# Kernel optimization log

Hardware: AMD Instinct MI355X
Metric: run time of the kernel (lower is better)

The kernel has to match this reference:

```python
import jax, jax.numpy as jnp
import numpy as np

N = 100000   # nodes
E = 1600000  # edges
F = 128      # in = out features
BN_EPS = 1e-5


def setup_inputs() -> dict:
    key = jax.random.key(0)
    ks = jax.random.split(key, 20)
    s = 1.0 / np.sqrt(F)
    inp = {
        "x": jax.random.normal(ks[0], (N, F), dtype=jnp.float32),
        "edge_index": jax.random.randint(ks[1], (2, E), 0, N, dtype=jnp.int64),
        "edge_type": jax.random.randint(ks[2], (E,), 0, 2, dtype=jnp.int64),
        # self-loop linear
        "w_sl": jax.random.normal(ks[3], (F, F), dtype=jnp.float32) * s,
        "b_sl": jnp.zeros((F,), dtype=jnp.float32),
        # GIN MLP for relation 0 (edge_type==0)
        "w1_n": jax.random.normal(ks[4], (F, F), dtype=jnp.float32) * s,
        "b1_n": jnp.zeros((F,), dtype=jnp.float32),
        "gamma_n": jnp.ones((F,), dtype=jnp.float32),
        "beta_n": jnp.zeros((F,), dtype=jnp.float32),
        "w2_n": jax.random.normal(ks[5], (F, F), dtype=jnp.float32) * s,
        "b2_n": jnp.zeros((F,), dtype=jnp.float32),
        # GIN MLP for relation 1 (edge_type==1)
        "w1_d": jax.random.normal(ks[6], (F, F), dtype=jnp.float32) * s,
        "b1_d": jnp.zeros((F,), dtype=jnp.float32),
        "gamma_d": jnp.ones((F,), dtype=jnp.float32),
        "beta_d": jnp.zeros((F,), dtype=jnp.float32),
        "w2_d": jax.random.normal(ks[7], (F, F), dtype=jnp.float32) * s,
        "b2_d": jnp.zeros((F,), dtype=jnp.float32),
        # gate linear: 3F -> F
        "w_gat": jax.random.normal(ks[8], (F, 3 * F), dtype=jnp.float32) * (1.0 / np.sqrt(3 * F)),
        "b_gat": jnp.zeros((F,), dtype=jnp.float32),
    }
    return inp


def _gin_branch(x, src, dst, mask, w1, b1, gamma, beta, w2, b2):
    # masked gather-scatter: equivalent to selecting edge columns with edge_type==r
    msg = x[src] * mask[:, None]                         # [E, F]
    agg = jax.ops.segment_sum(msg, dst, num_segments=N)  # [N, F]
    h = agg + x                                          # (1 + eps)*x with eps=0
    h = h @ w1.T + b1
    # BatchNorm1d, training-mode batch statistics (biased variance)
    mu = jnp.mean(h, axis=0)
    var = jnp.var(h, axis=0)
    h = gamma * (h - mu) * jax.lax.rsqrt(var + BN_EPS) + beta
    h = jax.nn.relu(h)
    return h @ w2.T + b2


def reference(x, edge_index, edge_type, w_sl, b_sl,
              w1_n, b1_n, gamma_n, beta_n, w2_n, b2_n,
              w1_d, b1_d, gamma_d, beta_d, w2_d, b2_d,
              w_gat, b_gat):
    src, dst = edge_index[0], edge_index[1]
    mask_n = (edge_type == 0).astype(x.dtype)
    mask_d = (edge_type == 1).astype(x.dtype)

    x_new_x = x @ w_sl.T + b_sl
    x_new_n = _gin_branch(x, src, dst, mask_n, w1_n, b1_n, gamma_n, beta_n, w2_n, b2_n)
    x_new_d = _gin_branch(x, src, dst, mask_d, w1_d, b1_d, gamma_d, beta_d, w2_d, b2_d)

    cat = jnp.concatenate((x_new_x, x_new_n, x_new_d), axis=1)   # [N, 3F]
    gat_raw = jax.nn.softmax(cat @ w_gat.T + b_gat, axis=-1)     # [N, F]
    gat = jnp.cumsum(gat_raw, axis=-1)
    out = (x_new_x + x_new_n) * (1.0 - gat) + (x_new_x + x_new_n + jnp.flip(x_new_d, axis=1)) * gat
    return out
```

## Files before the change

kernel.cpp:

```cpp
#include <hip/hip_runtime.h>
#include <stdint.h>

#define FF 128
#define MFMA __builtin_amdgcn_mfma_f32_16x16x32_bf16

typedef __attribute__((ext_vector_type(8))) short bf8_t;
typedef __attribute__((ext_vector_type(4))) float f4_t;
typedef __attribute__((ext_vector_type(8))) uint16_t us8_t;

__device__ __forceinline__ uint16_t f2bf(float f) {
  union { float f; uint32_t u; } v; v.f = f;
  return (uint16_t)((v.u + 0x7fffu + ((v.u >> 16) & 1u)) >> 16);
}
__device__ __forceinline__ float bf2f(uint16_t h) {
  union { uint32_t u; float f; } v; v.u = ((uint32_t)h) << 16;
  return v.f;
}

__device__ __forceinline__ void g2lds16(const void* g, void* l) {
  __builtin_amdgcn_global_load_lds(
      (const __attribute__((address_space(1))) uint32_t*)g,
      (__attribute__((address_space(3))) uint32_t*)l, 16, 0, 0);
}

#define STAGE_W8(Wp)                                                           \
  do {                                                                         \
    _Pragma("unroll") for (int j_ = 0; j_ < 4; ++j_) {                         \
      int k_ = j_ * 8 + w;                                                     \
      int r_ = ((k_ & 1) << 6) + lane;                                         \
      int c_ = k_ >> 1;                                                        \
      g2lds16((const char*)(Wp) + (size_t)r_ * 256 + c_ * 16,                  \
              (char*)wlds + k_ * 1024);                                        \
    }                                                                          \
  } while (0)

#define STAGE2(Wp, Gp)                                                         \
  do {                                                                         \
    _Pragma("unroll") for (int j_ = 0; j_ < 8; ++j_) {                         \
      int k_ = j_ * 8 + w;                                                     \
      int cc_ = k_ & 31;                                                       \
      const char* sp_ = (j_ < 4) ? (const char*)(Wp) : (const char*)(Gp);      \
      int r_ = ((cc_ & 1) << 6) + lane;                                        \
      int c_ = cc_ >> 1;                                                       \
      g2lds16(sp_ + (size_t)r_ * 256 + c_ * 16, (char*)wlds + k_ * 1024);      \
    }                                                                          \
  } while (0)

#define WFRAG(s, t) (*(const bf8_t*)&wlds[((s)*4 + lg) * 1024 + ((t)*16 + lr) * 8])
#define GFRAG(s, t) \
  (*(const bf8_t*)&wlds[16384 + ((s)*4 + lg) * 1024 + ((t)*16 + lr) * 8])

__global__ __launch_bounds__(256) void cvt_w_k(
    const float* __restrict__ wsl, const float* __restrict__ w1n,
    const float* __restrict__ w2n, const float* __restrict__ w1d,
    const float* __restrict__ w2d, uint16_t* __restrict__ o) {
  int i = blockIdx.x * 256 + threadIdx.x;
  if (i >= 5 * 16384) return;
  int wsel = i >> 14, j = i & 16383;
  const float* p = (wsel == 0) ? wsl : (wsel == 1) ? w1n : (wsel == 2) ? w2n
                   : (wsel == 3) ? w1d : w2d;
  o[i] = f2bf(p[j]);
}

__global__ __launch_bounds__(256) void gatepre_k(
    const float* __restrict__ wgat, const float* __restrict__ wsl,
    const float* __restrict__ w2n, const float* __restrict__ w2d,
    uint16_t* __restrict__ G) {
  const int mat = blockIdx.x >> 3;
  const int jblk = blockIdx.x & 7;
  const float* A = wgat + mat * 128;
  const float* B = (mat == 0) ? wsl : (mat == 1) ? w2n : w2d;
  const int i = threadIdx.x & 127;
  const int jo = jblk * 16 + (threadIdx.x >> 7) * 8;
  float acc[8] = {0.f, 0.f, 0.f, 0.f, 0.f, 0.f, 0.f, 0.f};
#pragma unroll 4
  for (int k = 0; k < 128; ++k) {
    float a = A[(size_t)i * 384 + k];
    const float* br = B + (size_t)k * 128 + jo;
#pragma unroll
    for (int j = 0; j < 8; ++j) acc[j] = fmaf(a, br[j], acc[j]);
  }
  uint16_t* g = G + mat * 16384 + i * 128 + jo;
#pragma unroll
  for (int j = 0; j < 8; ++j) g[j] = f2bf(acc[j]);
}

__global__ void bgatp_k(const float* __restrict__ wgat, const float* __restrict__ b_sl,
                        const float* __restrict__ b2n, const float* __restrict__ b2d,
                        const float* __restrict__ bgat, float* __restrict__ bgp) {
  int i = threadIdx.x;
  float s = bgat[i];
  for (int k = 0; k < 128; ++k) {
    s += wgat[(size_t)i * 384 + k] * b_sl[k];
    s += wgat[(size_t)i * 384 + 128 + k] * b2n[k];
    s += wgat[(size_t)i * 384 + 256 + k] * b2d[k];
  }
  bgp[i] = s;
}

__global__ __launch_bounds__(256) void cvt_x_k(const float* __restrict__ x,
                                               uint16_t* __restrict__ xb, int n4) {
  int i = blockIdx.x * 256 + threadIdx.x;
  if (i >= n4) return;
  float4 v = ((const float4*)x)[i];
  uint2 o;
  o.x = ((uint32_t)f2bf(v.y) << 16) | f2bf(v.x);
  o.y = ((uint32_t)f2bf(v.w) << 16) | f2bf(v.z);
  ((uint2*)xb)[i] = o;
}

__global__ __launch_bounds__(256) void hist_k(const int* __restrict__ dst,
                                              const int* __restrict__ ety,
                                              int* __restrict__ hist, int E) {
  int i = blockIdx.x * 256 + threadIdx.x;
  if (i < E) atomicAdd(&hist[(dst[i] << 1) | ety[i]], 1);
}

__global__ __launch_bounds__(256) void scan1_k(const int* __restrict__ hist,
                                               int* __restrict__ off,
                                               int* __restrict__ bsum, int nbins) {
  int i = blockIdx.x * 256 + threadIdx.x;
  int v = (i < nbins) ? hist[i] : 0;
  int lane = threadIdx.x & 63, w = threadIdx.x >> 6;
  int s = v;
#pragma unroll
  for (int d = 1; d < 64; d <<= 1) {
    int o = __shfl_up(s, (unsigned)d, 64);
    if (lane >= d) s += o;
  }
  __shared__ int wsum[4];
  if (lane == 63) wsum[w] = s;
  __syncthreads();
  int add = 0;
  for (int k = 0; k < w; ++k) add += wsum[k];
  s += add;
  if (i < nbins) off[i] = s - v;
  if (threadIdx.x == 255) bsum[blockIdx.x] = s;
}

__global__ __launch_bounds__(1024) void scan2_k(int* __restrict__ bsum, int nb) {
  int t = threadIdx.x;
  int v = (t < nb) ? bsum[t] : 0;
  int lane = t & 63, w = t >> 6;
  int s = v;
#pragma unroll
  for (int d = 1; d < 64; d <<= 1) {
    int o = __shfl_up(s, (unsigned)d, 64);
    if (lane >= d) s += o;
  }
  __shared__ int ws[16];
  if (lane == 63) ws[w] = s;
  __syncthreads();
  int add = 0;
  for (int k = 0; k < w; ++k) add += ws[k];
  s += add;
  if (t < nb) bsum[t] = s - v;
}

__global__ __launch_bounds__(256) void scan3_k(int* __restrict__ off,
                                               int* __restrict__ ccur,
                                               const int* __restrict__ bsum,
                                               int nbins, int E) {
  int i = blockIdx.x * 256 + threadIdx.x;
  if (i < nbins) {
    int v = off[i] + bsum[blockIdx.x];
    off[i] = v;
    if ((i & 511) == 0) ccur[i >> 9] = v;
  }
  if (i == nbins) off[i] = E;
}

#define BK_EPT 16
__global__ __launch_bounds__(256) void bucketize_k(const int* __restrict__ src,
                                                   const int* __restrict__ dst,
                                                   const int* __restrict__ ety,
                                                   int* __restrict__ ccur,
                                                   uint32_t* __restrict__ bk,
                                                   int E, int nbuckets) {
  __shared__ int lhist[512];
  __shared__ int lbase[512];
  const int tid = threadIdx.x;
  const int base = blockIdx.x * (256 * BK_EPT);
  for (int j = tid; j < nbuckets; j += 256) lhist[j] = 0;
  __syncthreads();

  uint32_t pk[BK_EPT];
  uint32_t rk[BK_EPT];
#pragma unroll
  for (int j = 0; j < BK_EPT; ++j) {
    int i = base + j * 256 + tid;
    if (i < E) {
      int bin = (dst[i] << 1) | ety[i];
      int bucket = bin >> 9;
      int rank = atomicAdd(&lhist[bucket], 1);
      pk[j] = (uint32_t)src[i] | ((uint32_t)(bin & 511) << 17);
      rk[j] = (uint32_t)bucket | ((uint32_t)rank << 9);
    } else {
      rk[j] = 0xFFFFFFFFu;
    }
  }
  __syncthreads();
  for (int j = tid; j < nbuckets; j += 256) {
    int c = lhist[j];
    lbase[j] = c ? atomicAdd(&ccur[j], c) : 0;
  }
  __syncthreads();
#pragma unroll
  for (int j = 0; j < BK_EPT; ++j) {
    if (rk[j] != 0xFFFFFFFFu) {
      int bucket = (int)(rk[j] & 511u);
      int rank = (int)(rk[j] >> 9);
      bk[lbase[bucket] + rank] = pk[j];
    }
  }
}

__global__ __launch_bounds__(256) void sctfine_k(const int* __restrict__ off,
                                                 const uint32_t* __restrict__ bk,
                                                 int* __restrict__ ssrc, int nbins) {
  __shared__ int lcur[512];
  const int b = blockIdx.x;
  const int binbase = b << 9;
  const int binend = min(binbase + 512, nbins);
  for (int j = threadIdx.x; j < binend - binbase; j += 256)
    lcur[j] = off[binbase + j];
  __syncthreads();
  const int estart = off[binbase], eend = off[binend];
  for (int i = estart + (int)threadIdx.x; i < eend; i += 256) {
    uint32_t pk = bk[i];
    int pos = atomicAdd(&lcur[pk >> 17], 1);
    ssrc[pos] = (int)(pk & 0x1FFFFu);
  }
}

__global__ __launch_bounds__(256) void agg_k(const int* __restrict__ off,
                                             const int* __restrict__ ssrc,
                                             const uint16_t* __restrict__ xb,
                                             uint16_t* __restrict__ xanb,
                                             uint16_t* __restrict__ xadb, int nbins) {
  int wid = (blockIdx.x * 256 + threadIdx.x) >> 6;
  int lane = threadIdx.x & 63;
  if (wid >= nbins) return;
  const int q = lane >> 4, c = lane & 15;
  int e = off[wid], end = off[wid + 1];
  float acc[8] = {0.f, 0.f, 0.f, 0.f, 0.f, 0.f, 0.f, 0.f};

#define ACC8(v)                                                       \
  do {                                                                \
    union { uint32_t u; float f; } lo_, hi_;                          \
    lo_.u = (v).x << 16; hi_.u = (v).x & 0xffff0000u;                 \
    acc[0] += lo_.f; acc[1] += hi_.f;                                 \
    lo_.u = (v).y << 16; hi_.u = (v).y & 0xffff0000u;                 \
    acc[2] += lo_.f; acc[3] += hi_.f;                                 \
    lo_.u = (v).z << 16; hi_.u = (v).z & 0xffff0000u;                 \
    acc[4] += lo_.f; acc[5] += hi_.f;                                 \
    lo_.u = (v).w << 16; hi_.u = (v).w & 0xffff0000u;                 \
    acc[6] += lo_.f; acc[7] += hi_.f;                                 \
  } while (0)

  for (; e + 8 <= end; e += 8) {
    int s0 = ssrc[e + q];
    int s1 = ssrc[e + 4 + q];
    uint4 v0 = *(const uint4*)(xb + (size_t)s0 * FF + c * 8);
    uint4 v1 = *(const uint4*)(xb + (size_t)s1 * FF + c * 8);
    ACC8(v0);
    ACC8(v1);
  }
  for (; e + 4 <= end; e += 4) {
    int s0 = ssrc[e + q];
    uint4 v0 = *(const uint4*)(xb + (size_t)s0 * FF + c * 8);
    ACC8(v0);
  }
  int r = end - e;
  if (r > 0) {
    int s0 = ssrc[e + min(q, r - 1)];
    uint4 v0 = *(const uint4*)(xb + (size_t)s0 * FF + c * 8);
    if (q < r) ACC8(v0);
  }
#undef ACC8

#pragma unroll
  for (int j = 0; j < 8; ++j) {
    acc[j] += __shfl_xor(acc[j], 16, 64);
    acc[j] += __shfl_xor(acc[j], 32, 64);
  }
  const int n = wid >> 1;
  uint4 own = *(const uint4*)(xb + (size_t)n * FF + c * 8);
  {
    union { uint32_t u; float f; } lo_, hi_;
    lo_.u = own.x << 16; hi_.u = own.x & 0xffff0000u;
    acc[0] += lo_.f; acc[1] += hi_.f;
    lo_.u = own.y << 16; hi_.u = own.y & 0xffff0000u;
    acc[2] += lo_.f; acc[3] += hi_.f;
    lo_.u = own.z << 16; hi_.u = own.z & 0xffff0000u;
    acc[4] += lo_.f; acc[5] += hi_.f;
    lo_.u = own.w << 16; hi_.u = own.w & 0xffff0000u;
    acc[6] += lo_.f; acc[7] += hi_.f;
  }
  if (q == 0) {
    uint4 o;
    o.x = ((uint32_t)f2bf(acc[1]) << 16) | f2bf(acc[0]);
    o.y = ((uint32_t)f2bf(acc[3]) << 16) | f2bf(acc[2]);
    o.z = ((uint32_t)f2bf(acc[5]) << 16) | f2bf(acc[4]);
    o.w = ((uint32_t)f2bf(acc[7]) << 16) | f2bf(acc[6]);
    uint16_t* dstp = (wid & 1) ? xadb : xanb;
    *(uint4*)(dstp + (size_t)n * FF + c * 8) = o;
  }
}

__global__ __launch_bounds__(512) void gemm1_k(
    const uint16_t* __restrict__ xanb, const uint16_t* __restrict__ xadb,
    const uint16_t* __restrict__ wbf, const float* __restrict__ b1n,
    const float* __restrict__ b1d, uint16_t* __restrict__ h1n,
    uint16_t* __restrict__ h1d, float* __restrict__ gstats, int N) {
  __shared__ __align__(16) uint16_t wlds[16384];
  __shared__ float sstat[8][4][128];
  const int tid = threadIdx.x;
  const int lane = tid & 63, w = tid >> 6;
  const int lr = lane & 15, lg = lane >> 4;
  const int rowbase = blockIdx.x * 256 + w * 32;
  const int arow0 = min(rowbase + lr, N - 1);
  const int arow1 = min(rowbase + 16 + lr, N - 1);

  f4_t acc[2][8];
  const f4_t zz = {0.f, 0.f, 0.f, 0.f};
  bf8_t a0[4], a1[4];

  STAGE_W8(wbf + 16384);
#pragma unroll
  for (int s = 0; s < 4; ++s) {
    const int k0 = s * 32 + lg * 8;
    a0[s] = *(const bf8_t*)(xanb + (size_t)arow0 * FF + k0);
    a1[s] = *(const bf8_t*)(xanb + (size_t)arow1 * FF + k0);
  }
  __syncthreads();

#pragma unroll 1
  for (int gi = 0; gi < 2; ++gi) {
#pragma unroll
    for (int rg = 0; rg < 2; ++rg)
#pragma unroll
      for (int t = 0; t < 8; ++t) acc[rg][t] = zz;
#pragma unroll
    for (int s = 0; s < 4; ++s) {
#pragma unroll
      for (int t = 0; t < 8; ++t) {
        bf8_t b = WFRAG(s, t);
        acc[0][t] = MFMA(a0[s], b, acc[0][t], 0, 0, 0);
        acc[1][t] = MFMA(a1[s], b, acc[1][t], 0, 0, 0);
      }
    }
    const float* bp = gi ? b1d : b1n;
    uint16_t* hp = gi ? h1d : h1n;
#pragma unroll
    for (int t = 0; t < 8; ++t) {
      const int col = t * 16 + lr;
      const float b = bp[col];
      float sum = 0.f, ss = 0.f;
#pragma unroll
      for (int rg = 0; rg < 2; ++rg)
#pragma unroll
        for (int r = 0; r < 4; ++r) {
          const int row = rowbase + rg * 16 + lg * 4 + r;
          const float h = acc[rg][t][r] + b;
          if (row < N) {
            hp[(size_t)row * FF + col] = f2bf(h);
            sum += h;
            ss += h * h;
          }
        }
      sum += __shfl_xor(sum, 16, 64);
      sum += __shfl_xor(sum, 32, 64);
      ss += __shfl_xor(ss, 16, 64);
      ss += __shfl_xor(ss, 32, 64);
      if (lane < 16) {
        sstat[w][gi * 2 + 0][col] = sum;
        sstat[w][gi * 2 + 1][col] = ss;
      }
    }
    if (gi == 0) {
      __syncthreads();
      STAGE_W8(wbf + 3 * 16384);
#pragma unroll
      for (int s = 0; s < 4; ++s) {
        const int k0 = s * 32 + lg * 8;
        a0[s] = *(const bf8_t*)(xadb + (size_t)arow0 * FF + k0);
        a1[s] = *(const bf8_t*)(xadb + (size_t)arow1 * FF + k0);
      }
      __syncthreads();
    }
  }
  __syncthreads();
  if (tid < 512) {
    int a = tid >> 7, c = tid & 127;
    float v = 0.f;
#pragma unroll
    for (int ww = 0; ww < 8; ++ww) v += sstat[ww][a][c];
    unsafeAtomicAdd(&gstats[tid], v);
  }
}

__global__ void bnfin_k(const float* __restrict__ gstats,
                        const float* __restrict__ gamn, const float* __restrict__ betn,
                        const float* __restrict__ gamd, const float* __restrict__ betd,
                        float* __restrict__ bnp, int N) {
  int i = threadIdx.x;
  float invN = 1.f / (float)N;
  {
    float mu = gstats[i] * invN;
    float var = gstats[128 + i] * invN - mu * mu;
    float sc = gamn[i] * rsqrtf(var + 1e-5f);
    bnp[i] = sc;
    bnp[128 + i] = betn[i] - mu * sc;
  }
  {
    float mu = gstats[256 + i] * invN;
    float var = gstats[384 + i] * invN - mu * mu;
    float sc = gamd[i] * rsqrtf(var + 1e-5f);
    bnp[256 + i] = sc;
    bnp[384 + i] = betd[i] - mu * sc;
  }
}

__global__ __launch_bounds__(512) void fuse2_k(
    const uint16_t* __restrict__ xb, const uint16_t* __restrict__ h1n,
    const uint16_t* __restrict__ h1d, const uint16_t* __restrict__ wbf,
    const uint16_t* __restrict__ G, const float* __restrict__ bnp,
    const float* __restrict__ b_sl, const float* __restrict__ b2n,
    const float* __restrict__ b2d, const float* __restrict__ bgp,
    float* __restrict__ out, int N) {
  __shared__ __align__(16) uint16_t wlds[32768];
  const int tid = threadIdx.x;
  const int lane = tid & 63, w = tid >> 6;
  const int lr = lane & 15, lg = lane >> 4;
  const int rowbase = blockIdx.x * 128 + w * 16;
  const int arow = min(rowbase + lr, N - 1);

  f4_t sum[8];
  f4_t accG[8];
  f4_t wk[8];
  const f4_t zz = {0.f, 0.f, 0.f, 0.f};

  STAGE2(wbf, G);

  bf8_t xa[4];
  us8_t hvn[4];
#pragma unroll
  for (int s = 0; s < 4; ++s) {
    const int k0 = s * 32 + lg * 8;
    xa[s] = *(const bf8_t*)(xb + (size_t)arow * FF + k0);
    hvn[s] = *(const us8_t*)(h1n + (size_t)arow * FF + k0);
  }
  __syncthreads();

#pragma unroll
  for (int t = 0; t < 8; ++t) { sum[t] = zz; accG[t] = zz; }
#pragma unroll
  for (int s = 0; s < 4; ++s) {
#pragma unroll
    for (int t = 0; t < 8; ++t) sum[t] = MFMA(xa[s], WFRAG(s, t), sum[t], 0, 0, 0);
#pragma unroll
    for (int t = 0; t < 8; ++t) accG[t] = MFMA(xa[s], GFRAG(s, t), accG[t], 0, 0, 0);
  }
#pragma unroll
  for (int t = 0; t < 8; ++t) {
    const float b = b_sl[t * 16 + lr];
#pragma unroll
    for (int r = 0; r < 4; ++r) sum[t][r] += b;
  }
  __syncthreads();

  STAGE2(wbf + 2 * 16384, G + 16384);
  us8_t hvd[4];
#pragma unroll
  for (int s = 0; s < 4; ++s)
    hvd[s] = *(const us8_t*)(h1d + (size_t)arow * FF + s * 32 + lg * 8);
  __syncthreads();

#pragma unroll
  for (int t = 0; t < 8; ++t) wk[t] = zz;
#pragma unroll
  for (int s = 0; s < 4; ++s) {
    const int k0 = s * 32 + lg * 8;
    f4_t sc0 = *(const f4_t*)(bnp + k0), sc1 = *(const f4_t*)(bnp + k0 + 4);
    f4_t sh0 = *(const f4_t*)(bnp + 128 + k0), sh1 = *(const f4_t*)(bnp + 128 + k0 + 4);
    bf8_t a;
#pragma unroll
    for (int j = 0; j < 4; ++j) {
      a[j] = (short)f2bf(fmaxf(bf2f(hvn[s][j]) * sc0[j] + sh0[j], 0.f));
      a[j + 4] = (short)f2bf(fmaxf(bf2f(hvn[s][j + 4]) * sc1[j] + sh1[j], 0.f));
    }
#pragma unroll
    for (int t = 0; t < 8; ++t) wk[t] = MFMA(a, WFRAG(s, t), wk[t], 0, 0, 0);
#pragma unroll
    for (int t = 0; t < 8; ++t) accG[t] = MFMA(a, GFRAG(s, t), accG[t], 0, 0, 0);
  }
#pragma unroll
  for (int t = 0; t < 8; ++t) {
    const float b = b2n[t * 16 + lr];
#pragma unroll
    for (int r = 0; r < 4; ++r) sum[t][r] += wk[t][r] + b;
  }
  __syncthreads();

  STAGE2(wbf + 4 * 16384, G + 2 * 16384);
  __syncthreads();

#pragma unroll
  for (int t = 0; t < 8; ++t) wk[t] = zz;
#pragma unroll
  for (int s = 0; s < 4; ++s) {
    const int k0 = s * 32 + lg * 8;
    const float* bnb = bnp + 256;
    f4_t sc0 = *(const f4_t*)(bnb + k0), sc1 = *(const f4_t*)(bnb + k0 + 4);
    f4_t sh0 = *(const f4_t*)(bnb + 128 + k0), sh1 = *(const f4_t*)(bnb + 128 + k0 + 4);
    bf8_t a;
#pragma unroll
    for (int j = 0; j < 4; ++j) {
      a[j] = (short)f2bf(fmaxf(bf2f(hvd[s][j]) * sc0[j] + sh0[j], 0.f));
      a[j + 4] = (short)f2bf(fmaxf(bf2f(hvd[s][j + 4]) * sc1[j] + sh1[j], 0.f));
    }
#pragma unroll
    for (int t = 0; t < 8; ++t) wk[t] = MFMA(a, WFRAG(s, t), wk[t], 0, 0, 0);
#pragma unroll
    for (int t = 0; t < 8; ++t) accG[t] = MFMA(a, GFRAG(s, t), accG[t], 0, 0, 0);
  }
#pragma unroll
  for (int t = 0; t < 8; ++t) {
    const float b = b2d[t * 16 + lr];
#pragma unroll
    for (int r = 0; r < 4; ++r) wk[t][r] += b;
  }

  float bg[8];
#pragma unroll
  for (int t = 0; t < 8; ++t) bg[t] = bgp[t * 16 + lr];
#pragma unroll
  for (int r = 0; r < 4; ++r) {
    float lv[8];
#pragma unroll
    for (int t = 0; t < 8; ++t) lv[t] = accG[t][r] + bg[t];
    float m = lv[0];
#pragma unroll
    for (int t = 1; t < 8; ++t) m = fmaxf(m, lv[t]);
#pragma unroll
    for (int d = 1; d < 16; d <<= 1) m = fmaxf(m, __shfl_xor(m, d, 16));
    float g[8];
    float run = 0.f;
#pragma unroll
    for (int t = 0; t < 8; ++t) {
      float p = __expf(lv[t] - m);
      float scn = p;
#pragma unroll
      for (int d = 1; d < 16; d <<= 1) {
        float o = __shfl_up(scn, (unsigned)d, 16);
        if (lr >= d) scn += o;
      }
      g[t] = run + scn;
      run += __shfl(scn, 15, 16);
    }
    const float inv = 1.f / run;
    float xdf[8];
#pragma unroll
    for (int t = 0; t < 8; ++t) xdf[t] = __shfl_xor(wk[7 - t][r], 15, 64);
    const int row = rowbase + lg * 4 + r;
    if (row < N) {
#pragma unroll
      for (int t = 0; t < 8; ++t)
        out[(size_t)row * FF + t * 16 + lr] = sum[t][r] + xdf[t] * (g[t] * inv);
    }
  }
}

extern "C" void kernel_launch(void* const* d_in, const int* in_sizes, int n_in,
                              void* d_out, int out_size, void* d_ws, size_t ws_size,
                              hipStream_t stream) {
  const float* x = (const float*)d_in[0];
  const int* eidx = (const int*)d_in[1];
  const int* etype = (const int*)d_in[2];
  const float* w_sl = (const float*)d_in[3];
  const float* b_sl = (const float*)d_in[4];
  const float* w1n = (const float*)d_in[5];
  const float* b1n = (const float*)d_in[6];
  const float* gamn = (const float*)d_in[7];
  const float* betn = (const float*)d_in[8];
  const float* w2n = (const float*)d_in[9];
  const float* b2n = (const float*)d_in[10];
  const float* w1d = (const float*)d_in[11];
  const float* b1d = (const float*)d_in[12];
  const float* gamd = (const float*)d_in[13];
  const float* betd = (const float*)d_in[14];
  const float* w2d = (const float*)d_in[15];
  const float* b2d = (const float*)d_in[16];
  const float* wgat = (const float*)d_in[17];
  const float* bgat = (const float*)d_in[18];
  float* out = (float*)d_out;

  const int N = in_sizes[0] / FF;
  const int E = in_sizes[2];
  const int* src = eidx;
  const int* dst = eidx + E;
  const int nbins = 2 * N;
  const int nbuckets = (nbins + 511) >> 9;

  const size_t NF = (size_t)N * FF;
  float* gstats = (float*)d_ws;
  float* bnp = gstats + 512;
  float* bgp = bnp + 512;
  uint16_t* wbf = (uint16_t*)(bgp + 128);
  uint16_t* G = wbf + 5 * 16384;
  uint16_t* xb = G + 3 * 16384;
  uint16_t* xanb = xb + NF;
  uint16_t* xadb = xanb + NF;
  uint16_t* h1n = xadb + NF;
  uint16_t* h1d = h1n + NF;
  int* hist = (int*)(h1d + NF);
  int* off = hist + nbins;
  int* ccur = off + nbins + 1;
  int* bsum = ccur + nbuckets;
  int* ssrc = bsum + 1024;
  uint32_t* bk = (uint32_t*)(ssrc + E);

  const int nb1 = (nbins + 255) / 256;

  hipMemsetAsync(hist, 0, (size_t)nbins * sizeof(int), stream);
  hipMemsetAsync(gstats, 0, 512 * sizeof(float), stream);
  cvt_w_k<<<320, 256, 0, stream>>>(w_sl, w1n, w2n, w1d, w2d, wbf);
  cvt_x_k<<<(int)((NF / 4 + 255) / 256), 256, 0, stream>>>(x, xb, (int)(NF / 4));
  gatepre_k<<<24, 256, 0, stream>>>(wgat, w_sl, w2n, w2d, G);
  bgatp_k<<<1, 128, 0, stream>>>(wgat, b_sl, b2n, b2d, bgat, bgp);

  hist_k<<<(E + 255) / 256, 256, 0, stream>>>(dst, etype, hist, E);
  scan1_k<<<nb1, 256, 0, stream>>>(hist, off, bsum, nbins);
  scan2_k<<<1, 1024, 0, stream>>>(bsum, nb1);
  scan3_k<<<(nbins + 256) / 256, 256, 0, stream>>>(off, ccur, bsum, nbins, E);
  bucketize_k<<<(E + 256 * BK_EPT - 1) / (256 * BK_EPT), 256, 0, stream>>>(
      src, dst, etype, ccur, bk, E, nbuckets);
  sctfine_k<<<nbuckets, 256, 0, stream>>>(off, bk, ssrc, nbins);
  agg_k<<<(nbins + 3) / 4, 256, 0, stream>>>(off, ssrc, xb, xanb, xadb, nbins);

  gemm1_k<<<(N + 255) / 256, 512, 0, stream>>>(xanb, xadb, wbf, b1n, b1d, h1n, h1d,
                                               gstats, N);
  bnfin_k<<<1, 128, 0, stream>>>(gstats, gamn, betn, gamd, betd, bnp, N);
  fuse2_k<<<(N + 127) / 128, 512, 0, stream>>>(xb, h1n, h1d, wbf, G, bnp, b_sl,
                                               b2n, b2d, bgp, out, N);
}
```

Before: 381.2 us.

## Process two row tiles per wave in fuse2 and reorder branches to cut registers

fuse2_k now handles 256 rows per block, with each wave computing two 16-row MFMA tiles. Each weight fragment read from LDS is reused for both tiles, which halves the weight staging and LDS reads per row. The d-branch runs first and its result is packed into bf16 registers, and the self-loop and n-branch then share one accumulator with their biases pre-summed. This keeps register pressure down despite the doubled tile. The trade-off is fewer blocks and possibly lower occupancy, plus an extra bf16 rounding of the d-branch output.

```diff
diff --git a/kernel.cpp b/kernel.cpp
--- a/kernel.cpp
+++ b/kernel.cpp
@@ -15,6 +15,9 @@
 __device__ __forceinline__ float bf2f(uint16_t h) {
   union { uint32_t u; float f; } v; v.u = ((uint32_t)h) << 16;
   return v.f;
+}
+__device__ __forceinline__ uint32_t pk2bf(float a, float b) {
+  return ((uint32_t)f2bf(b) << 16) | f2bf(a);
 }
 
 __device__ __forceinline__ void g2lds16(const void* g, void* l) {
@@ -299,10 +302,10 @@
   }
   if (q == 0) {
     uint4 o;
-    o.x = ((uint32_t)f2bf(acc[1]) << 16) | f2bf(acc[0]);
-    o.y = ((uint32_t)f2bf(acc[3]) << 16) | f2bf(acc[2]);
-    o.z = ((uint32_t)f2bf(acc[5]) << 16) | f2bf(acc[4]);
-    o.w = ((uint32_t)f2bf(acc[7]) << 16) | f2bf(acc[6]);
+    o.x = pk2bf(acc[0], acc[1]);
+    o.y = pk2bf(acc[2], acc[3]);
+    o.z = pk2bf(acc[4], acc[5]);
+    o.w = pk2bf(acc[6], acc[7]);
     uint16_t* dstp = (wid & 1) ? xadb : xanb;
     *(uint4*)(dstp + (size_t)n * FF + c * 8) = o;
   }
@@ -433,141 +436,183 @@
   const int tid = threadIdx.x;
   const int lane = tid & 63, w = tid >> 6;
   const int lr = lane & 15, lg = lane >> 4;
-  const int rowbase = blockIdx.x * 128 + w * 16;
-  const int arow = min(rowbase + lr, N - 1);
-
-  f4_t sum[8];
-  f4_t accG[8];
-  f4_t wk[8];
+  const int rowbase = blockIdx.x * 256 + w * 32;
+  const int arow0 = min(rowbase + lr, N - 1);
+  const int arow1 = min(rowbase + 16 + lr, N - 1);
+
+  f4_t accG[2][8];
+  f4_t wk[2][8];
+  uint2 xdp[2][8];
   const f4_t zz = {0.f, 0.f, 0.f, 0.f};
 
-  STAGE2(wbf, G);
-
-  bf8_t xa[4];
-  us8_t hvn[4];
+  STAGE2(wbf + 4 * 16384, G + 2 * 16384);
+  us8_t hv0[4], hv1[4];
 #pragma unroll
   for (int s = 0; s < 4; ++s) {
     const int k0 = s * 32 + lg * 8;
-    xa[s] = *(const bf8_t*)(xb + (size_t)arow * FF + k0);
-    hvn[s] = *(const us8_t*)(h1n + (size_t)arow * FF + k0);
-  }
-  __syncthreads();
-
-#pragma unroll
-  for (int t = 0; t < 8; ++t) { sum[t] = zz; accG[t] = zz; }
+    hv0[s] = *(const us8_t*)(h1d + (size_t)arow0 * FF + k0);
+    hv1[s] = *(const us8_t*)(h1d + (size_t)arow1 * FF + k0);
+  }
+  __syncthreads();
+
+#pragma unroll
+  for (int t = 0; t < 8; ++t) {
+    wk[0][t] = zz; wk[1][t] = zz;
+    accG[0][t] = zz; accG[1][t] = zz;
+  }
+  {
+    const float* bnb = bnp + 256;
+#pragma unroll
+    for (int s = 0; s < 4; ++s) {
+      const int k0 = s * 32 + lg * 8;
+      f4_t sc0 = *(const f4_t*)(bnb + k0), sc1 = *(const f4_t*)(bnb + k0 + 4);
+      f4_t sh0 = *(const f4_t*)(bnb + 128 + k0), sh1 = *(const f4_t*)(bnb + 128 + k0 + 4);
+      bf8_t a0, a1;
+#pragma unroll
+      for (int j = 0; j < 4; ++j) {
+        a0[j] = (short)f2bf(fmaxf(bf2f(hv0[s][j]) * sc0[j] + sh0[j], 0.f));
+        a0[j + 4] = (short)f2bf(fmaxf(bf2f(hv0[s][j + 4]) * sc1[j] + sh1[j], 0.f));
+        a1[j] = (short)f2bf(fmaxf(bf2f(hv1[s][j]) * sc0[j] + sh0[j], 0.f));
+        a1[j + 4] = (short)f2bf(fmaxf(bf2f(hv1[s][j + 4]) * sc1[j] + sh1[j], 0.f));
+      }
+#pragma unroll
+      for (int t = 0; t < 8; ++t) {
+        bf8_t b = WFRAG(s, t);
+        wk[0][t] = MFMA(a0, b, wk[0][t], 0, 0, 0);
+        wk[1][t] = MFMA(a1, b, wk[1][t], 0, 0, 0);
+      }
+#pragma unroll
+      for (int t = 0; t < 8; ++t) {
+        bf8_t b = GFRAG(s, t);
+        accG[0][t] = MFMA(a0, b, accG[0][t], 0, 0, 0);
+        accG[1][t] = MFMA(a1, b, accG[1][t], 0, 0, 0);
+      }
+    }
+  }
+#pragma unroll
+  for (int t = 0; t < 8; ++t) {
+    const float bd = b2d[t * 16 + lr];
+#pragma unroll
+    for (int rg = 0; rg < 2; ++rg) {
+      xdp[rg][t].x = pk2bf(wk[rg][t][0] + bd, wk[rg][t][1] + bd);
+      xdp[rg][t].y = pk2bf(wk[rg][t][2] + bd, wk[rg][t][3] + bd);
+    }
+  }
+  __syncthreads();
+
+  STAGE2(wbf, G);
+  bf8_t xa0[4], xa1[4];
 #pragma unroll
   for (int s = 0; s < 4; ++s) {
-#pragma unroll
-    for (int t = 0; t < 8; ++t) sum[t] = MFMA(xa[s], WFRAG(s, t), sum[t], 0, 0, 0);
-#pragma unroll
-    for (int t = 0; t < 8; ++t) accG[t] = MFMA(xa[s], GFRAG(s, t), accG[t], 0, 0, 0);
-  }
-#pragma unroll
-  for (int t = 0; t < 8; ++t) {
-    const float b = b_sl[t * 16 + lr];
-#pragma unroll
-    for (int r = 0; r < 4; ++r) sum[t][r] += b;
+    const int k0 = s * 32 + lg * 8;
+    xa0[s] = *(const bf8_t*)(xb + (size_t)arow0 * FF + k0);
+    xa1[s] = *(const bf8_t*)(xb + (size_t)arow1 * FF + k0);
+  }
+  __syncthreads();
+
+#pragma unroll
+  for (int t = 0; t < 8; ++t) { wk[0][t] = zz; wk[1][t] = zz; }
+#pragma unroll
+  for (int s = 0; s < 4; ++s) {
+#pragma unroll
+    for (int t = 0; t < 8; ++t) {
+      bf8_t b = WFRAG(s, t);
+      wk[0][t] = MFMA(xa0[s], b, wk[0][t], 0, 0, 0);
+      wk[1][t] = MFMA(xa1[s], b, wk[1][t], 0, 0, 0);
+    }
+#pragma unroll
+    for (int t = 0; t < 8; ++t) {
+      bf8_t b = GFRAG(s, t);
+      accG[0][t] = MFMA(xa0[s], b, accG[0][t], 0, 0, 0);
+      accG[1][t] = MFMA(xa1[s], b, accG[1][t], 0, 0, 0);
+    }
   }
   __syncthreads();
 
   STAGE2(wbf + 2 * 16384, G + 16384);
-  us8_t hvd[4];
-#pragma unroll
-  for (int s = 0; s < 4; ++s)
-    hvd[s] = *(const us8_t*)(h1d + (size_t)arow * FF + s * 32 + lg * 8);
-  __syncthreads();
-
-#pragma unroll
-  for (int t = 0; t < 8; ++t) wk[t] = zz;
+#pragma unroll
+  for (int s = 0; s < 4; ++s) {
+    const int k0 = s * 32 + lg * 8;
+    hv0[s] = *(const us8_t*)(h1n + (size_t)arow0 * FF + k0);
+    hv1[s] = *(const us8_t*)(h1n + (size_t)arow1 * FF + k0);
+  }
+  __syncthreads();
+
 #pragma unroll
   for (int s = 0; s < 4; ++s) {
     const int k0 = s * 32 + lg * 8;
     f4_t sc0 = *(const f4_t*)(bnp + k0), sc1 = *(const f4_t*)(bnp + k0 + 4);
     f4_t sh0 = *(const f4_t*)(bnp + 128 + k0), sh1 = *(const f4_t*)(bnp + 128 + k0 + 4);
-    bf8_t a;
+    bf8_t a0, a1;
 #pragma unroll
     for (int j = 0; j < 4; ++j) {
-      a[j] = (short)f2bf(fmaxf(bf2f(hvn[s][j]) * sc0[j] + sh0[j], 0.f));
-      a[j + 4] = (short)f2bf(fmaxf(bf2f(hvn[s][j + 4]) * sc1[j] + sh1[j], 0.f));
-    }
-#pragma unroll
-    for (int t = 0; t < 8; ++t) wk[t] = MFMA(a, WFRAG(s, t), wk[t], 0, 0, 0);
-#pragma unroll
-    for (int t = 0; t < 8; ++t) accG[t] = MFMA(a, GFRAG(s, t), accG[t], 0, 0, 0);
-  }
+      a0[j] = (short)f2bf(fmaxf(bf2f(hv0[s][j]) * sc0[j] + sh0[j], 0.f));
+      a0[j + 4] = (short)f2bf(fmaxf(bf2f(hv0[s][j + 4]) * sc1[j] + sh1[j], 0.f));
+      a1[j] = (short)f2bf(fmaxf(bf2f(hv1[s][j]) * sc0[j] + sh0[j], 0.f));
+      a1[j + 4] = (short)f2bf(fmaxf(bf2f(hv1[s][j + 4]) * sc1[j] + sh1[j], 0.f));
+    }
+#pragma unroll
+    for (int t = 0; t < 8; ++t) {
+      bf8_t b = WFRAG(s, t);
+      wk[0][t] = MFMA(a0, b, wk[0][t], 0, 0, 0);
+      wk[1][t] = MFMA(a1, b, wk[1][t], 0, 0, 0);
+    }
+#pragma unroll
+    for (int t = 0; t < 8; ++t) {
+      bf8_t b = GFRAG(s, t);
+      accG[0][t] = MFMA(a0, b, accG[0][t], 0, 0, 0);
+      accG[1][t] = MFMA(a1, b, accG[1][t], 0, 0, 0);
+    }
+  }
+
+  float bg[8], bb[8];
 #pragma unroll
   for (int t = 0; t < 8; ++t) {
-    const float b = b2n[t * 16 + lr];
-#pragma unroll
-    for (int r = 0; r < 4; ++r) sum[t][r] += wk[t][r] + b;
-  }
-  __syncthreads();
-
-  STAGE2(wbf + 4 * 16384, G + 2 * 16384);
-  __syncthreads();
-
-#pragma unroll
-  for (int t = 0; t < 8; ++t) wk[t] = zz;
-#pragma unroll
-  for (int s = 0; s < 4; ++s) {
-    const int k0 = s * 32 + lg * 8;
-    const float* bnb = bnp + 256;
-    f4_t sc0 = *(const f4_t*)(bnb + k0), sc1 = *(const f4_t*)(bnb + k0 + 4);
-    f4_t sh0 = *(const f4_t*)(bnb + 128 + k0), sh1 = *(const f4_t*)(bnb + 128 + k0 + 4);
-    bf8_t a;
-#pragma unroll
-    for (int j = 0; j < 4; ++j) {
-      a[j] = (short)f2bf(fmaxf(bf2f(hvd[s][j]) * sc0[j] + sh0[j], 0.f));
-      a[j + 4] = (short)f2bf(fmaxf(bf2f(hvd[s][j + 4]) * sc1[j] + sh1[j], 0.f));
-    }
-#pragma unroll
-    for (int t = 0; t < 8; ++t) wk[t] = MFMA(a, WFRAG(s, t), wk[t], 0, 0, 0);
-#pragma unroll
-    for (int t = 0; t < 8; ++t) accG[t] = MFMA(a, GFRAG(s, t), accG[t], 0, 0, 0);
-  }
-#pragma unroll
-  for (int t = 0; t < 8; ++t) {
-    const float b = b2d[t * 16 + lr];
-#pragma unroll
-    for (int r = 0; r < 4; ++r) wk[t][r] += b;
-  }
-
-  float bg[8];
-#pragma unroll
-  for (int t = 0; t < 8; ++t) bg[t] = bgp[t * 16 + lr];
-#pragma unroll
-  for (int r = 0; r < 4; ++r) {
-    float lv[8];
-#pragma unroll
-    for (int t = 0; t < 8; ++t) lv[t] = accG[t][r] + bg[t];
-    float m = lv[0];
-#pragma unroll
-    for (int t = 1; t < 8; ++t) m = fmaxf(m, lv[t]);
-#pragma unroll
-    for (int d = 1; d < 16; d <<= 1) m = fmaxf(m, __shfl_xor(m, d, 16));
-    float g[8];
-    float run = 0.f;
-#pragma unroll
-    for (int t = 0; t < 8; ++t) {
-      float p = __expf(lv[t] - m);
-      float scn = p;
-#pragma unroll
-      for (int d = 1; d < 16; d <<= 1) {
-        float o = __shfl_up(scn, (unsigned)d, 16);
-        if (lr >= d) scn += o;
-      }
-      g[t] = run + scn;
-      run += __shfl(scn, 15, 16);
-    }
-    const float inv = 1.f / run;
-    float xdf[8];
-#pragma unroll
-    for (int t = 0; t < 8; ++t) xdf[t] = __shfl_xor(wk[7 - t][r], 15, 64);
-    const int row = rowbase + lg * 4 + r;
-    if (row < N) {
-#pragma unroll
-      for (int t = 0; t < 8; ++t)
-        out[(size_t)row * FF + t * 16 + lr] = sum[t][r] + xdf[t] * (g[t] * inv);
+    const int col = t * 16 + lr;
+    bg[t] = bgp[col];
+    bb[t] = b_sl[col] + b2n[col];
+  }
+#pragma unroll 1
+  for (int rg = 0; rg < 2; ++rg) {
+#pragma unroll
+    for (int r = 0; r < 4; ++r) {
+      float lv[8];
+#pragma unroll
+      for (int t = 0; t < 8; ++t) lv[t] = accG[rg][t][r] + bg[t];
+      float m = lv[0];
+#pragma unroll
+      for (int t = 1; t < 8; ++t) m = fmaxf(m, lv[t]);
+#pragma unroll
+      for (int d = 1; d < 16; d <<= 1) m = fmaxf(m, __shfl_xor(m, d, 16));
+      float g[8];
+      float run = 0.f;
+#pragma unroll
+      for (int t = 0; t < 8; ++t) {
+        float p = __expf(lv[t] - m);
+        float scn = p;
+#pragma unroll
+        for (int d = 1; d < 16; d <<= 1) {
+          float o = __shfl_up(scn, (unsigned)d, 16);
+          if (lr >= d) scn += o;
+        }
+        g[t] = run + scn;
+        run += __shfl(scn, 15, 16);
+      }
+      const float inv = 1.f / run;
+      float xdf[8];
+#pragma unroll
+      for (int t = 0; t < 8; ++t) {
+        uint32_t v = (r & 2) ? xdp[rg][7 - t].y : xdp[rg][7 - t].x;
+        uint32_t sv = (uint32_t)__shfl_xor((int)v, 15, 64);
+        xdf[t] = bf2f((uint16_t)((r & 1) ? (sv >> 16) : (sv & 0xffffu)));
+      }
+      const int row = rowbase + rg * 16 + lg * 4 + r;
+      if (row < N) {
+#pragma unroll
+        for (int t = 0; t < 8; ++t)
+          out[(size_t)row * FF + t * 16 + lr] =
+              wk[rg][t][r] + bb[t] + xdf[t] * (g[t] * inv);
+      }
     }
   }
 }
@@ -642,6 +687,6 @@
   gemm1_k<<<(N + 255) / 256, 512, 0, stream>>>(xanb, xadb, wbf, b1n, b1d, h1n, h1d,
                                                gstats, N);
   bnfin_k<<<1, 128, 0, stream>>>(gstats, gamn, betn, gamd, betd, bnp, N);
-  fuse2_k<<<(N + 127) / 128, 512, 0, stream>>>(xb, h1n, h1d, wbf, G, bnp, b_sl,
+  fuse2_k<<<(N + 255) / 256, 512, 0, stream>>>(xb, h1n, h1d, wbf, G, bnp, b_sl,
                                                b2n, b2d, bgp, out, N);
 }
```

Result: slower. 470.9 us (+23.5%).
